# Kernel optimization log

Measured on AMD Instinct MI355X. Metric: run time of the kernel, lower is better.

The kernel has to match this reference:

```python
import jax, jax.numpy as jnp
import numpy as np

B = 256       # batch size
D = 128       # dim_s == dim_t == inputSize
OUT = 1000000 # outputSize (memory bank rows)
K = 511       # number of negatives (idx has K+1 columns)
MOM = 0.5     # momentum


def setup_inputs() -> dict:
    key = jax.random.key(0)
    ks = jax.random.split(key, 18)
    stdv = 1.0 / np.sqrt(D / 3.0)
    sc = 1.0 / np.sqrt(D)  # nn.Linear default init bound
    inp = {}
    inp["v1"] = jax.random.normal(ks[0], (B, D), jnp.float32)
    inp["v2"] = jax.random.normal(ks[1], (B, D), jnp.float32)
    y = jax.random.randint(ks[2], (B,), 0, OUT)
    inp["y"] = y
    idx = jax.random.randint(ks[3], (B, K + 1), 0, OUT)
    inp["idx"] = idx.at[:, 0].set(y)  # first column is the positive, as in torch
    inp["memory_v1"] = jax.random.uniform(ks[4], (OUT, D), jnp.float32, -stdv, stdv)
    inp["memory_v2"] = jax.random.uniform(ks[5], (OUT, D), jnp.float32, -stdv, stdv)
    names = ["Ws1", "bs1", "Ws2", "bs2", "Wsv", "bsv", "Wt1", "bt1", "Wt2", "bt2", "Wtv", "btv"]
    for i, n in enumerate(names):
        shape = (D, D) if n.startswith("W") else (D,)
        inp[n] = jax.random.uniform(ks[6 + i], shape, jnp.float32, -sc, sc)
    return inp


def _branch(v, w2, W1, b1, W2, b2, Wv, bv):
    # v: [B, D], w2: [K+1, B, D] (gathered memory rows, detached)
    a = v @ W1.T + b1                                 # [B, D]
    b_ = jnp.einsum('kbd,ed->kbe', w2, W2) + b2       # [K+1, B, D]
    h = jax.nn.relu(a[None, :, :] - b_)               # [K+1, B, D]
    return jnp.einsum('kbd,ed->kbe', h, Wv) + bv      # [K+1, B, D]


def reference(v1, v2, y, idx, memory_v1, memory_v2,
              Ws1, bs1, Ws2, bs2, Wsv, bsv, Wt1, bt1, Wt2, bt2, Wtv, btv):
    # gather K+1 memory rows per sample (detached in torch)
    w2 = jax.lax.stop_gradient(memory_v2[idx])        # [B, K+1, D]
    w2 = jnp.transpose(w2, (1, 0, 2))                 # [K+1, B, D]

    outs_s = _branch(v1, w2, Ws1, bs1, Ws2, bs2, Wsv, bsv)  # stacked outs_m_t_s
    outs_t = _branch(v2, w2, Wt1, bt1, Wt2, bt2, Wtv, btv)  # stacked outs_m_t

    # momentum normalize-and-scatter update (torch.no_grad block)
    def upd(mem, v):
        rows = mem[y] * MOM + v * (1.0 - MOM)                     # [B, D]
        rows = rows / jnp.sqrt(jnp.sum(rows * rows, axis=1, keepdims=True))
        return mem.at[y].set(rows)

    new_mem_v1 = jax.lax.stop_gradient(upd(memory_v1, v1))
    new_mem_v2 = jax.lax.stop_gradient(upd(memory_v2, v2))

    # torch returns (outs_m_t, outs_m_t_s) as lists; we stack them along K+1,
    # and additionally return the updated memory banks (the buffer side effect).
    return outs_t, outs_s, new_mem_v1, new_mem_v2
```

## Files before the change

### kernel.cpp

```cpp
#include <hip/hip_runtime.h>


typedef __attribute__((ext_vector_type(8))) short bf16x8;
typedef __attribute__((ext_vector_type(4))) float f32x4;

__device__ __forceinline__ unsigned short f2bf(float f) {
    union { float ff; unsigned u; } v; v.ff = f;
    unsigned u = v.u;
    u += 0x7fffu + ((u >> 16) & 1u);
    return (unsigned short)(u >> 16);
}

__global__ void prep_weights(const float* __restrict__ Ws2,
                             const float* __restrict__ Wsv,
                             const float* __restrict__ Wt2,
                             const float* __restrict__ Wtv,
                             unsigned short* __restrict__ wb) {
    int i = blockIdx.x * 256 + threadIdx.x;
    if (i < 16384) {
        wb[i]         = f2bf(Ws2[i]);
        wb[16384 + i] = f2bf(Wsv[i]);
        wb[32768 + i] = f2bf(Wt2[i]);
        wb[49152 + i] = f2bf(Wtv[i]);
    }
}

__global__ void prep_a(const float* __restrict__ v1, const float* __restrict__ v2,
                       const float* __restrict__ Ws1, const float* __restrict__ bs1,
                       const float* __restrict__ bs2,
                       const float* __restrict__ Wt1, const float* __restrict__ bt1,
                       const float* __restrict__ bt2,
                       float* __restrict__ aS, float* __restrict__ aT) {
    __shared__ float vs1[128], vs2[128];
    const int b = blockIdx.x, e = threadIdx.x;
    vs1[e] = v1[b * 128 + e];
    vs2[e] = v2[b * 128 + e];
    __syncthreads();
    float s1 = 0.f, s2 = 0.f;
    const float4* w1 = (const float4*)(Ws1 + e * 128);
    const float4* w2 = (const float4*)(Wt1 + e * 128);
    #pragma unroll
    for (int d4 = 0; d4 < 32; ++d4) {
        float4 a = w1[d4], c = w2[d4];
        s1 += a.x * vs1[d4*4] + a.y * vs1[d4*4+1] + a.z * vs1[d4*4+2] + a.w * vs1[d4*4+3];
        s2 += c.x * vs2[d4*4] + c.y * vs2[d4*4+1] + c.z * vs2[d4*4+2] + c.w * vs2[d4*4+3];
    }
    aS[b * 128 + e] = s1 + bs1[e] - bs2[e];
    aT[b * 128 + e] = s2 + bt1[e] - bt2[e];
}

__global__ __launch_bounds__(256) void branch_fused(
    const float* __restrict__ memv2, const int* __restrict__ idx,
    const float* __restrict__ aS, const float* __restrict__ aT,
    const unsigned short* __restrict__ wb,
    const float* __restrict__ bsv, const float* __restrict__ btv,
    float* __restrict__ outT, float* __restrict__ outS)
{
    __shared__ unsigned short Xs[128 * 128];
    __shared__ unsigned short Ht[128 * 128];

    const int tid  = threadIdx.x;
    const int wv   = tid >> 6, lane = tid & 63;
    const int m0   = blockIdx.x * 128;
    const int b0   = m0 & 255;
    const int kq   = m0 >> 8;

    {
        const int sub = lane >> 5;
        const int c4  = (lane & 31) * 4;
        #pragma unroll
        for (int i = 0; i < 16; ++i) {
            const int r = wv * 32 + i * 2 + sub;
            const int grow = idx[(b0 + r) * 512 + kq];
            const float4 x = *(const float4*)(memv2 + (long)grow * 128 + c4);
            ushort4 u;
            u.x = f2bf(x.x); u.y = f2bf(x.y); u.z = f2bf(x.z); u.w = f2bf(x.w);
            *(ushort4*)&Xs[r * 128 + (c4 ^ ((r & 7) * 8))] = u;
        }
    }
    __syncthreads();

    const int r0   = wv * 32;
    const int lrow = lane & 15;
    const int kg   = lane >> 4;

    const unsigned short* Ws2b = wb;
    const unsigned short* Wsvb = wb + 16384;
    const unsigned short* Wt2b = wb + 32768;
    const unsigned short* Wtvb = wb + 49152;

    f32x4 accS[2][8], accT[2][8];
    #pragma unroll
    for (int mf = 0; mf < 2; ++mf)
        #pragma unroll
        for (int nf = 0; nf < 8; ++nf) {
            accS[mf][nf] = (f32x4){0.f, 0.f, 0.f, 0.f};
            accT[mf][nf] = (f32x4){0.f, 0.f, 0.f, 0.f};
        }

    #pragma unroll
    for (int kk = 0; kk < 4; ++kk) {
        const int kb = kk * 32 + kg * 8;
        const int ra = r0 + lrow, rb = r0 + 16 + lrow;
        bf16x8 A0 = *(const bf16x8*)&Xs[ra * 128 + (kb ^ ((ra & 7) * 8))];
        bf16x8 A1 = *(const bf16x8*)&Xs[rb * 128 + (kb ^ ((rb & 7) * 8))];
        #pragma unroll
        for (int nf = 0; nf < 8; ++nf) {
            const int e = nf * 16 + lrow;
            bf16x8 Bs = *(const bf16x8*)&Ws2b[e * 128 + kb];
            bf16x8 Bt = *(const bf16x8*)&Wt2b[e * 128 + kb];
            accS[0][nf] = __builtin_amdgcn_mfma_f32_16x16x32_bf16(A0, Bs, accS[0][nf], 0, 0, 0);
            accS[1][nf] = __builtin_amdgcn_mfma_f32_16x16x32_bf16(A1, Bs, accS[1][nf], 0, 0, 0);
            accT[0][nf] = __builtin_amdgcn_mfma_f32_16x16x32_bf16(A0, Bt, accT[0][nf], 0, 0, 0);
            accT[1][nf] = __builtin_amdgcn_mfma_f32_16x16x32_bf16(A1, Bt, accT[1][nf], 0, 0, 0);
        }
    }
    __syncthreads();

    #pragma unroll
    for (int mf = 0; mf < 2; ++mf) {
        #pragma unroll
        for (int nf = 0; nf < 8; ++nf) {
            const int e = nf * 16 + lrow;
            #pragma unroll
            for (int j = 0; j < 4; ++j) {
                const int rt = r0 + mf * 16 + kg * 4 + j;
                const int b  = b0 + rt;
                float hS = fmaxf(aS[b * 128 + e] - accS[mf][nf][j], 0.f);
                float hT = fmaxf(aT[b * 128 + e] - accT[mf][nf][j], 0.f);
                const int ei = e ^ ((rt & 7) * 8);
                Xs[rt * 128 + ei] = f2bf(hS);
                Ht[rt * 128 + ei] = f2bf(hT);
            }
        }
    }
    __syncthreads();

    f32x4 oS[2][8], oT[2][8];
    #pragma unroll
    for (int mf = 0; mf < 2; ++mf)
        #pragma unroll
        for (int nf = 0; nf < 8; ++nf) {
            oS[mf][nf] = (f32x4){0.f, 0.f, 0.f, 0.f};
            oT[mf][nf] = (f32x4){0.f, 0.f, 0.f, 0.f};
        }
    #pragma unroll
    for (int kk = 0; kk < 4; ++kk) {
        const int kb = kk * 32 + kg * 8;
        const int ra = r0 + lrow, rb = r0 + 16 + lrow;
        bf16x8 AS0 = *(const bf16x8*)&Xs[ra * 128 + (kb ^ ((ra & 7) * 8))];
        bf16x8 AS1 = *(const bf16x8*)&Xs[rb * 128 + (kb ^ ((rb & 7) * 8))];
        bf16x8 AT0 = *(const bf16x8*)&Ht[ra * 128 + (kb ^ ((ra & 7) * 8))];
        bf16x8 AT1 = *(const bf16x8*)&Ht[rb * 128 + (kb ^ ((rb & 7) * 8))];
        #pragma unroll
        for (int nf = 0; nf < 8; ++nf) {
            const int e = nf * 16 + lrow;
            bf16x8 Bs = *(const bf16x8*)&Wsvb[e * 128 + kb];
            bf16x8 Bt = *(const bf16x8*)&Wtvb[e * 128 + kb];
            oS[0][nf] = __builtin_amdgcn_mfma_f32_16x16x32_bf16(AS0, Bs, oS[0][nf], 0, 0, 0);
            oS[1][nf] = __builtin_amdgcn_mfma_f32_16x16x32_bf16(AS1, Bs, oS[1][nf], 0, 0, 0);
            oT[0][nf] = __builtin_amdgcn_mfma_f32_16x16x32_bf16(AT0, Bt, oT[0][nf], 0, 0, 0);
            oT[1][nf] = __builtin_amdgcn_mfma_f32_16x16x32_bf16(AT1, Bt, oT[1][nf], 0, 0, 0);
        }
    }

    float bvS[8], bvT[8];
    #pragma unroll
    for (int nf = 0; nf < 8; ++nf) {
        bvS[nf] = bsv[nf * 16 + lrow];
        bvT[nf] = btv[nf * 16 + lrow];
    }
    #pragma unroll
    for (int mf = 0; mf < 2; ++mf) {
        #pragma unroll
        for (int nf = 0; nf < 8; ++nf) {
            const int e = nf * 16 + lrow;
            #pragma unroll
            for (int j = 0; j < 4; ++j) {
                const int rt = r0 + mf * 16 + kg * 4 + j;
                const long off = (long)(m0 + rt) * 128 + e;
                outT[off] = oT[mf][nf][j] + bvT[nf];
                outS[off] = oS[mf][nf][j] + bvS[nf];
            }
        }
    }
}

__global__ void update_mem(const float* __restrict__ v1, const float* __restrict__ v2,
                           const int* __restrict__ y,
                           const float* __restrict__ m1, const float* __restrict__ m2,
                           float* __restrict__ o1, float* __restrict__ o2) {
    __shared__ int s_skip;
    __shared__ float part1[2], part2[2];
    const int b = blockIdx.x, t = threadIdx.x;
    const int yb = y[b];
    if (t == 0) {
        int sk = 0;
        for (int b2 = b + 1; b2 < 256; ++b2) sk |= (y[b2] == yb);
        s_skip = sk;
    }
    __syncthreads();
    if (s_skip) return;
    float x1 = m1[(long)yb * 128 + t] * 0.5f + v1[b * 128 + t] * 0.5f;
    float x2 = m2[(long)yb * 128 + t] * 0.5f + v2[b * 128 + t] * 0.5f;
    float s1 = x1 * x1, s2 = x2 * x2;
    #pragma unroll
    for (int o = 32; o > 0; o >>= 1) {
        s1 += __shfl_down(s1, o);
        s2 += __shfl_down(s2, o);
    }
    if ((t & 63) == 0) { part1[t >> 6] = s1; part2[t >> 6] = s2; }
    __syncthreads();
    const float n1 = part1[0] + part1[1];
    const float n2 = part2[0] + part2[1];
    o1[(long)yb * 128 + t] = x1 / sqrtf(n1);
    o2[(long)yb * 128 + t] = x2 / sqrtf(n2);
}

extern "C" void kernel_launch(void* const* d_in, const int* in_sizes, int n_in,
                              void* d_out, int out_size, void* d_ws, size_t ws_size,
                              hipStream_t stream) {
    (void)in_sizes; (void)n_in; (void)out_size; (void)ws_size;
    const float* v1  = (const float*)d_in[0];
    const float* v2  = (const float*)d_in[1];
    const int*   y   = (const int*)d_in[2];
    const int*   idx = (const int*)d_in[3];
    const float* mv1 = (const float*)d_in[4];
    const float* mv2 = (const float*)d_in[5];
    const float* Ws1 = (const float*)d_in[6];
    const float* bs1 = (const float*)d_in[7];
    const float* Ws2 = (const float*)d_in[8];
    const float* bs2 = (const float*)d_in[9];
    const float* Wsv = (const float*)d_in[10];
    const float* bsv = (const float*)d_in[11];
    const float* Wt1 = (const float*)d_in[12];
    const float* bt1 = (const float*)d_in[13];
    const float* Wt2 = (const float*)d_in[14];
    const float* bt2 = (const float*)d_in[15];
    const float* Wtv = (const float*)d_in[16];
    const float* btv = (const float*)d_in[17];

    float* outT = (float*)d_out;
    float* outS = outT + 16777216;
    float* oM1  = outT + 33554432;
    float* oM2  = oM1 + 128000000;

    float* aS = (float*)d_ws;
    float* aT = aS + 32768;
    unsigned short* wb = (unsigned short*)(aT + 32768);

    prep_weights<<<64, 256, 0, stream>>>(Ws2, Wsv, Wt2, Wtv, wb);
    prep_a<<<256, 128, 0, stream>>>(v1, v2, Ws1, bs1, bs2, Wt1, bt1, bt2, aS, aT);
    branch_fused<<<1024, 256, 0, stream>>>(mv2, idx, aS, aT, wb, bsv, btv, outT, outS);
    hipMemcpyAsync(oM1, mv1, 128000000ull * sizeof(float), hipMemcpyDeviceToDevice, stream);
    hipMemcpyAsync(oM2, mv2, 128000000ull * sizeof(float), hipMemcpyDeviceToDevice, stream);
    update_mem<<<256, 128, 0, stream>>>(v1, v2, y, mv1, mv2, oM1, oM2);
}
```

Before: 533.4 us.

## Fuse memory-bank copies into branch kernel as interleaved copy blocks

Replaces the two hipMemcpyAsync device-to-device copies and the separate branch kernel with one launch, where every third block runs the gather/MFMA branch work and the other blocks copy chunks of the memory banks. The intent is to overlap the bandwidth-bound 1 GB bank copy with the compute-heavy branch and to drop the copy-engine/launch overhead. It also makes output stores nontemporal and uses nontemporal loads for bank1, which is not re-read, while keeping normal loads for bank2 so gathered rows may stay cached. The risk is that the large shared-memory footprint declared for copy blocks lowers occupancy for the copy work.

```diff
diff --git a/kernel.cpp b/kernel.cpp
--- a/kernel.cpp
+++ b/kernel.cpp
@@ -3,6 +3,7 @@
 
 typedef __attribute__((ext_vector_type(8))) short bf16x8;
 typedef __attribute__((ext_vector_type(4))) float f32x4;
+typedef __attribute__((ext_vector_type(4))) float fvec4;
 
 __device__ __forceinline__ unsigned short f2bf(float f) {
     union { float ff; unsigned u; } v; v.ff = f;
@@ -49,19 +50,18 @@
     aT[b * 128 + e] = s2 + bt1[e] - bt2[e];
 }
 
-__global__ __launch_bounds__(256) void branch_fused(
+__device__ __forceinline__ void branch_body(
+    int blk,
     const float* __restrict__ memv2, const int* __restrict__ idx,
     const float* __restrict__ aS, const float* __restrict__ aT,
     const unsigned short* __restrict__ wb,
     const float* __restrict__ bsv, const float* __restrict__ btv,
-    float* __restrict__ outT, float* __restrict__ outS)
+    float* __restrict__ outT, float* __restrict__ outS,
+    unsigned short* Xs, unsigned short* Ht)
 {
-    __shared__ unsigned short Xs[128 * 128];
-    __shared__ unsigned short Ht[128 * 128];
-
     const int tid  = threadIdx.x;
     const int wv   = tid >> 6, lane = tid & 63;
-    const int m0   = blockIdx.x * 128;
+    const int m0   = blk * 128;
     const int b0   = m0 & 255;
     const int kq   = m0 >> 8;
 
@@ -179,10 +179,55 @@
             for (int j = 0; j < 4; ++j) {
                 const int rt = r0 + mf * 16 + kg * 4 + j;
                 const long off = (long)(m0 + rt) * 128 + e;
-                outT[off] = oT[mf][nf][j] + bvT[nf];
-                outS[off] = oS[mf][nf][j] + bvS[nf];
+                __builtin_nontemporal_store(oT[mf][nf][j] + bvT[nf], outT + off);
+                __builtin_nontemporal_store(oS[mf][nf][j] + bvS[nf], outS + off);
             }
         }
+    }
+}
+
+__device__ __forceinline__ void copy_body(
+    int cid, const float* __restrict__ mv1, const float* __restrict__ mv2,
+    float* __restrict__ oM1, float* __restrict__ oM2)
+{
+    const bool bank2 = (cid >= 1000);
+    const long base = (long)(bank2 ? cid - 1000 : cid) * 32000;
+    const fvec4* src = (bank2 ? (const fvec4*)mv2 : (const fvec4*)mv1) + base;
+    fvec4* dst = (bank2 ? (fvec4*)oM2 : (fvec4*)oM1) + base;
+    const int t = threadIdx.x;
+    #pragma unroll 1
+    for (int i = 0; i < 125; i += 5) {
+        fvec4 v[5];
+        #pragma unroll
+        for (int u = 0; u < 5; ++u) {
+            const fvec4* p = src + (long)(i + u) * 256 + t;
+            v[u] = bank2 ? *p : __builtin_nontemporal_load(p);
+        }
+        #pragma unroll
+        for (int u = 0; u < 5; ++u)
+            __builtin_nontemporal_store(v[u], dst + (long)(i + u) * 256 + t);
+    }
+}
+
+__global__ __launch_bounds__(256) void mega(
+    const float* __restrict__ memv2, const int* __restrict__ idx,
+    const float* __restrict__ aS, const float* __restrict__ aT,
+    const unsigned short* __restrict__ wb,
+    const float* __restrict__ bsv, const float* __restrict__ btv,
+    float* __restrict__ outT, float* __restrict__ outS,
+    const float* __restrict__ mv1,
+    float* __restrict__ oM1, float* __restrict__ oM2)
+{
+    __shared__ unsigned short Xs[128 * 128];
+    __shared__ unsigned short Ht[128 * 128];
+    const int bid = blockIdx.x;
+    const int r3 = bid % 3;
+    if (r3 == 0) {
+        branch_body(bid / 3, memv2, idx, aS, aT, wb, bsv, btv, outT, outS, Xs, Ht);
+    } else {
+        const int cid = (bid / 3) * 2 + (r3 - 1);
+        if (cid < 2000)
+            copy_body(cid, mv1, memv2, oM1, oM2);
     }
 }
 
@@ -251,8 +296,7 @@
 
     prep_weights<<<64, 256, 0, stream>>>(Ws2, Wsv, Wt2, Wtv, wb);
     prep_a<<<256, 128, 0, stream>>>(v1, v2, Ws1, bs1, bs2, Wt1, bt1, bt2, aS, aT);
-    branch_fused<<<1024, 256, 0, stream>>>(mv2, idx, aS, aT, wb, bsv, btv, outT, outS);
-    hipMemcpyAsync(oM1, mv1, 128000000ull * sizeof(float), hipMemcpyDeviceToDevice, stream);
-    hipMemcpyAsync(oM2, mv2, 128000000ull * sizeof(float), hipMemcpyDeviceToDevice, stream);
+    mega<<<3072, 256, 0, stream>>>(mv2, idx, aS, aT, wb, bsv, btv, outT, outS,
+                                   mv1, oM1, oM2);
     update_mem<<<256, 128, 0, stream>>>(v1, v2, y, mv1, mv2, oM1, oM2);
 }
```

Measured after the change: 461.7 us, median of 4. 1.16x faster.

## Fuse memory-bank copies into branch kernel, interleaved with compute phases

Applied to the files above, without the earlier changes.

The two device-to-device memcpys of the memory banks are replaced by in-kernel copy spans. Each of the 1024 blocks copies two 128K-float chunks, and the spans are interleaved between the gather, MFMA and epilogue phases so that bulk bandwidth work overlaps with compute. The copies and the final output stores use nontemporal loads and stores. The __syncthreads barriers are removed, which relies on each wave only reading LDS rows it wrote itself. The added copy code raises register pressure and may disturb the MFMA phases.

```diff
diff --git a/kernel.cpp b/kernel.cpp
--- a/kernel.cpp
+++ b/kernel.cpp
@@ -3,6 +3,7 @@
 
 typedef __attribute__((ext_vector_type(8))) short bf16x8;
 typedef __attribute__((ext_vector_type(4))) float f32x4;
+typedef __attribute__((ext_vector_type(4))) float fvec4;
 
 __device__ __forceinline__ unsigned short f2bf(float f) {
     union { float ff; unsigned u; } v; v.ff = f;
@@ -49,21 +50,54 @@
     aT[b * 128 + e] = s2 + bt1[e] - bt2[e];
 }
 
-__global__ __launch_bounds__(256) void branch_fused(
+__device__ __forceinline__ void copy_span(const fvec4* __restrict__ src,
+                                          fvec4* __restrict__ dst,
+                                          int t, int i0, int i1, bool cached) {
+    #pragma unroll 1
+    for (int i = i0; i < i1; i += 5) {
+        fvec4 v[5];
+        #pragma unroll
+        for (int u = 0; u < 5; ++u) {
+            const fvec4* p = src + (long)(i + u) * 256 + t;
+            v[u] = cached ? *p : __builtin_nontemporal_load(p);
+        }
+        #pragma unroll
+        for (int u = 0; u < 5; ++u)
+            __builtin_nontemporal_store(v[u], dst + (long)(i + u) * 256 + t);
+    }
+}
+
+__global__ __launch_bounds__(256) void mega(
     const float* __restrict__ memv2, const int* __restrict__ idx,
     const float* __restrict__ aS, const float* __restrict__ aT,
     const unsigned short* __restrict__ wb,
     const float* __restrict__ bsv, const float* __restrict__ btv,
-    float* __restrict__ outT, float* __restrict__ outS)
+    float* __restrict__ outT, float* __restrict__ outS,
+    const float* __restrict__ mv1,
+    float* __restrict__ oM1, float* __restrict__ oM2)
 {
     __shared__ unsigned short Xs[128 * 128];
     __shared__ unsigned short Ht[128 * 128];
 
+    const int bid  = blockIdx.x;
     const int tid  = threadIdx.x;
     const int wv   = tid >> 6, lane = tid & 63;
-    const int m0   = blockIdx.x * 128;
+    const int m0   = bid * 128;
     const int b0   = m0 & 255;
     const int kq   = m0 >> 8;
+    const int t    = tid;
+
+    const int c0 = bid * 2, c1 = bid * 2 + 1;
+    const bool has0 = c0 < 2000, has1 = c1 < 2000;
+    const bool b2_0 = c0 >= 1000, b2_1 = c1 >= 1000;
+    const long base0 = (long)(b2_0 ? c0 - 1000 : c0) * 32000;
+    const long base1 = (long)(b2_1 ? c1 - 1000 : c1) * 32000;
+    const fvec4* src0 = (b2_0 ? (const fvec4*)memv2 : (const fvec4*)mv1) + base0;
+    fvec4*       dst0 = (b2_0 ? (fvec4*)oM2 : (fvec4*)oM1) + base0;
+    const fvec4* src1 = (b2_1 ? (const fvec4*)memv2 : (const fvec4*)mv1) + base1;
+    fvec4*       dst1 = (b2_1 ? (fvec4*)oM2 : (fvec4*)oM1) + base1;
+
+    if (has0) copy_span(src0, dst0, t, 0, 25, b2_0);
 
     {
         const int sub = lane >> 5;
@@ -78,7 +112,8 @@
             *(ushort4*)&Xs[r * 128 + (c4 ^ ((r & 7) * 8))] = u;
         }
     }
-    __syncthreads();
+
+    if (has0) copy_span(src0, dst0, t, 25, 50, b2_0);
 
     const int r0   = wv * 32;
     const int lrow = lane & 15;
@@ -115,7 +150,8 @@
             accT[1][nf] = __builtin_amdgcn_mfma_f32_16x16x32_bf16(A1, Bt, accT[1][nf], 0, 0, 0);
         }
     }
-    __syncthreads();
+
+    if (has0) copy_span(src0, dst0, t, 50, 75, b2_0);
 
     #pragma unroll
     for (int mf = 0; mf < 2; ++mf) {
@@ -134,7 +170,8 @@
             }
         }
     }
-    __syncthreads();
+
+    if (has0) copy_span(src0, dst0, t, 75, 100, b2_0);
 
     f32x4 oS[2][8], oT[2][8];
     #pragma unroll
@@ -179,11 +216,14 @@
             for (int j = 0; j < 4; ++j) {
                 const int rt = r0 + mf * 16 + kg * 4 + j;
                 const long off = (long)(m0 + rt) * 128 + e;
-                outT[off] = oT[mf][nf][j] + bvT[nf];
-                outS[off] = oS[mf][nf][j] + bvS[nf];
+                __builtin_nontemporal_store(oT[mf][nf][j] + bvT[nf], outT + off);
+                __builtin_nontemporal_store(oS[mf][nf][j] + bvS[nf], outS + off);
             }
         }
     }
+
+    if (has0) copy_span(src0, dst0, t, 100, 125, b2_0);
+    if (has1) copy_span(src1, dst1, t, 0, 125, b2_1);
 }
 
 __global__ void update_mem(const float* __restrict__ v1, const float* __restrict__ v2,
@@ -251,8 +291,7 @@
 
     prep_weights<<<64, 256, 0, stream>>>(Ws2, Wsv, Wt2, Wtv, wb);
     prep_a<<<256, 128, 0, stream>>>(v1, v2, Ws1, bs1, bs2, Wt1, bt1, bt2, aS, aT);
-    branch_fused<<<1024, 256, 0, stream>>>(mv2, idx, aS, aT, wb, bsv, btv, outT, outS);
-    hipMemcpyAsync(oM1, mv1, 128000000ull * sizeof(float), hipMemcpyDeviceToDevice, stream);
-    hipMemcpyAsync(oM2, mv2, 128000000ull * sizeof(float), hipMemcpyDeviceToDevice, stream);
+    mega<<<1024, 256, 0, stream>>>(mv2, idx, aS, aT, wb, bsv, btv, outT, outS,
+                                   mv1, oM1, oM2);
     update_mem<<<256, 128, 0, stream>>>(v1, v2, y, mv1, mv2, oM1, oM2);
 }
```

After: 505.2 us. -5.3%, faster.
